# Performance work log

Measured on AMD Instinct MI355X. Metric: run time of the kernel, lower is better.

The kernel has to match this reference:

```python
import jax, jax.numpy as jnp
import numpy as np

B, T, I, H = 64, 512, 512, 512


def setup_inputs() -> dict:
    key = jax.random.key(0)
    ks = jax.random.split(key, 7)
    scale_i = 1.0 / np.sqrt(I)
    scale_h = 1.0 / np.sqrt(H)
    x = jax.random.normal(ks[0], (B, T, I), dtype=jnp.float32)
    h0 = jax.random.normal(ks[1], (B, H), dtype=jnp.float32)
    W_ih = jax.random.normal(ks[2], (3 * H, I), dtype=jnp.float32) * scale_i
    W_hh = jax.random.normal(ks[3], (3 * H, H), dtype=jnp.float32) * scale_h
    b_ih = jax.random.normal(ks[4], (3 * H,), dtype=jnp.float32) * scale_h
    b_hh = jax.random.normal(ks[5], (3 * H,), dtype=jnp.float32) * scale_h
    # ragged lengths, sorted descending (module's slicing logic assumes this)
    lengths = jnp.sort(jax.random.randint(ks[6], (B,), 1, T + 1))[::-1].astype(jnp.int64)
    return {"x": x, "h0": h0, "W_ih": W_ih, "W_hh": W_hh,
            "b_ih": b_ih, "b_hh": b_hh, "lengths": lengths}


def _gru_scan(x, h0, W_ih, W_hh, b_ih, b_hh, lengths):
    # Precompute input projections for all timesteps: [B, T, 3H]
    gi = jnp.einsum('bti,gi->btg', x, W_ih) + b_ih
    lengths = lengths.astype(jnp.int32)

    def step(h, inp):
        gi_t, t = inp  # gi_t: [B, 3H]
        gh = h @ W_hh.T + b_hh  # [B, 3H]
        i_r, i_z, i_n = jnp.split(gi_t, 3, axis=-1)
        h_r, h_z, h_n = jnp.split(gh, 3, axis=-1)
        r = jax.nn.sigmoid(i_r + h_r)
        z = jax.nn.sigmoid(i_z + h_z)
        n = jnp.tanh(i_n + r * h_n)
        h_new = (1.0 - z) * n + z * h
        m = (t < lengths)[:, None]  # ragged mask: valid rows this step
        h_keep = jnp.where(m, h_new, h)        # past-length rows keep last state
        y = jnp.where(m, h_new, 0.0)           # output stays zero past length
        return h_keep, y

    ts = jnp.arange(x.shape[1], dtype=jnp.int32)
    h_final, ys = jax.lax.scan(step, h0, (gi.transpose(1, 0, 2), ts))
    output = ys.transpose(1, 0, 2)  # [B, T, H]
    return output, h_final


def reference(x, h0, W_ih, W_hh, b_ih, b_hh, lengths):
    output, h_final = _gru_scan(x, h0, W_ih, W_hh, b_ih, b_hh, lengths)
    final_state = (h_final[None],)  # (1, B, H), matching unsqueeze(0)
    return output, final_state
```

## Files before the change

kernel.cpp:

```cpp
#include <hip/hip_runtime.h>
#include <stdint.h>

#define Bsz 64
#define Tsz 512
#define HD  512
#define GROUPS 4
#define MEMBERS 16
#define BROWS 16
#define JCH 32
#define NWG (GROUPS*MEMBERS)
#define NTHR 512
#define LROW 520
#define LROWD 260
#define HSLOT (Bsz*HD/2)

typedef __attribute__((ext_vector_type(8))) short bf16x8;
typedef __attribute__((ext_vector_type(4))) float f32x4;
typedef __attribute__((ext_vector_type(4))) uint32_t u32x4;
typedef __attribute__((ext_vector_type(2))) uint32_t u32x2;

#define BAR() asm volatile("s_waitcnt lgkmcnt(0)\n\ts_barrier" ::: "memory")

__device__ __forceinline__ uint32_t f2bf(float f) {
  uint32_t u = __builtin_bit_cast(uint32_t, f);
  return (u + 0x7FFFu + ((u >> 16) & 1u)) >> 16;
}

__device__ __forceinline__ bf16x8 ldwf(const float* __restrict__ W, int row, int k0) {
  const f32x4 a = *reinterpret_cast<const f32x4*>(W + (size_t)row * HD + k0);
  const f32x4 b = *reinterpret_cast<const f32x4*>(W + (size_t)row * HD + k0 + 4);
  bf16x8 r;
  r[0] = (short)f2bf(a.x); r[1] = (short)f2bf(a.y);
  r[2] = (short)f2bf(a.z); r[3] = (short)f2bf(a.w);
  r[4] = (short)f2bf(b.x); r[5] = (short)f2bf(b.y);
  r[6] = (short)f2bf(b.z); r[7] = (short)f2bf(b.w);
  return r;
}

__device__ __forceinline__ void stage_x0(const float* __restrict__ x, int b0,
                                         uint32_t* xl, int tid) {
#pragma unroll
  for (int i = 0; i < 4; ++i) {
    const int fl = tid + i * 512;
    const int row = fl >> 7;
    const int c4 = fl & 127;
    const f32x4 v = *reinterpret_cast<const f32x4*>(
        x + (size_t)(b0 + row) * Tsz * HD + c4 * 4);
    u32x2 w;
    w.x = f2bf(v.x) | (f2bf(v.y) << 16);
    w.y = f2bf(v.z) | (f2bf(v.w) << 16);
    *reinterpret_cast<u32x2*>(xl + row * LROWD + c4 * 2) = w;
  }
}

__global__ void gru_init(const float* __restrict__ h0, uint32_t* __restrict__ flg,
                         uint64_t* __restrict__ hbx) {
  const int i = blockIdx.x * 256 + threadIdx.x;
  if (i < 2 * GROUPS * 16) flg[i] = (i < GROUPS * 16) ? 0xFFFFFFFFu : 0u;
  if (i < HSLOT) {
    const float a = h0[2 * i], b = h0[2 * i + 1];
    hbx[HSLOT + i] = (uint64_t)(f2bf(a) | (f2bf(b) << 16));
    hbx[i] = 0xFFFFFFFF00000000ull;
  }
}

__global__ void __launch_bounds__(NTHR) gru_persist(
    const float* __restrict__ x, const float* __restrict__ h0,
    const float* __restrict__ Wih, const float* __restrict__ Whh,
    const float* __restrict__ bih, const float* __restrict__ bhh,
    const int* __restrict__ lens,
    float* __restrict__ out, float* __restrict__ outh,
    uint32_t* __restrict__ flg, uint64_t* __restrict__ hbx) {
  __shared__ alignas(16) unsigned short x_lds[2][BROWS * LROW];
  __shared__ alignas(16) unsigned short h_lds[BROWS * LROW];
  __shared__ alignas(16) float s_lds[BROWS][4][JCH];

  const int tid = threadIdx.x;
  const int lane = tid & 63;
  const int wv = tid >> 6;
  const int gid = blockIdx.x & 3;
  const int mem = blockIdx.x >> 2;
  const int b0 = gid * BROWS;
  const int j0 = mem * JCH;

  const int grow = tid >> 5;
  const int gj = tid & 31;
  const float br = bih[j0 + gj] + bhh[j0 + gj];
  const float bz = bih[512 + j0 + gj] + bhh[512 + j0 + gj];
  const float bi_n = bih[1024 + j0 + gj];
  const float bh_n = bhh[1024 + j0 + gj];
  float hprev = h0[(size_t)(b0 + grow) * HD + j0 + gj];
  const int lenr = lens[b0 + grow];
  float* const outp = out + (size_t)(b0 + grow) * Tsz * HD + j0 + gj;

  const int q = tid & 127;
  const int r0 = tid >> 7;

  const int xc4 = tid & 127;
  const int xr0 = tid >> 7;
  const float* xbp[4];
#pragma unroll
  for (int i = 0; i < 4; ++i)
    xbp[i] = x + (size_t)(b0 + xr0 + 4 * i) * Tsz * HD + xc4 * 4;

  const int c = lane & 15;
  const int kg = lane >> 4;
  bf16x8 wfa[16], wfb[16];
  if (wv < 4) {
    const int wrow = (wv >> 1) * 512 + j0 + (wv & 1) * 16 + c;
#pragma unroll
    for (int ks = 0; ks < 16; ++ks) {
      const int k0 = ks * 32 + kg * 8;
      wfa[ks] = ldwf(Wih, wrow, k0);
      wfb[ks] = ldwf(Whh, wrow, k0);
    }
  } else if (wv < 6) {
    const int wrow = 1024 + j0 + (wv - 4) * 16 + c;
#pragma unroll
    for (int ks = 0; ks < 16; ++ks) wfa[ks] = ldwf(Wih, wrow, ks * 32 + kg * 8);
  } else {
    const int wrow = 1024 + j0 + (wv - 6) * 16 + c;
#pragma unroll
    for (int ks = 0; ks < 16; ++ks) wfb[ks] = ldwf(Whh, wrow, ks * 32 + kg * 8);
  }

  stage_x0(x, b0, (uint32_t*)&x_lds[0][0], tid);

  f32x4 xr[4];
#pragma unroll
  for (int i = 0; i < 4; ++i)
    xr[i] = *reinterpret_cast<const f32x4*>(xbp[i] + (size_t)1 * HD);

  float o_pend = 0.f;

  __syncthreads();

  for (int t = 0; t < Tsz; ++t) {
    const uint32_t want = (uint32_t)t;
    const uint64_t* bp = hbx + (size_t)((t + 1) & 1) * HSLOT;
    const uint64_t* a0 = bp + (size_t)(b0 + r0) * 256 + q * 2;
    const uint64_t* a1 = a0 + 4 * 256;
    const uint64_t* a2 = a0 + 8 * 256;
    const uint64_t* a3 = a0 + 12 * 256;
    u32x4 d0, d1, d2, d3;

    asm volatile(
        "global_load_dwordx4 %0, %4, off sc0 sc1\n\t"
        "global_load_dwordx4 %1, %5, off sc0 sc1\n\t"
        "global_load_dwordx4 %2, %6, off sc0 sc1\n\t"
        "global_load_dwordx4 %3, %7, off sc0 sc1"
        : "=&v"(d0), "=&v"(d1), "=&v"(d2), "=&v"(d3)
        : "v"(a0), "v"(a1), "v"(a2), "v"(a3)
        : "memory");

    f32x4 acc0 = {0.f, 0.f, 0.f, 0.f}, acc1 = {0.f, 0.f, 0.f, 0.f};
    {
      const unsigned short* xl = &x_lds[t & 1][0];
      if (wv < 6) {
#pragma unroll
        for (int ks = 0; ks < 16; ks += 2) {
          bf16x8 a0f = *reinterpret_cast<const bf16x8*>(xl + c * LROW + ks * 32 + kg * 8);
          bf16x8 a1f = *reinterpret_cast<const bf16x8*>(xl + c * LROW + (ks + 1) * 32 + kg * 8);
          acc0 = __builtin_amdgcn_mfma_f32_16x16x32_bf16(a0f, wfa[ks], acc0, 0, 0, 0);
          acc1 = __builtin_amdgcn_mfma_f32_16x16x32_bf16(a1f, wfa[ks + 1], acc1, 0, 0, 0);
        }
      }
    }

    if (t + 1 < Tsz) {
      uint32_t* xl = (uint32_t*)&x_lds[(t + 1) & 1][0];
#pragma unroll
      for (int i = 0; i < 4; ++i) {
        u32x2 w;
        w.x = f2bf(xr[i].x) | (f2bf(xr[i].y) << 16);
        w.y = f2bf(xr[i].z) | (f2bf(xr[i].w) << 16);
        *reinterpret_cast<u32x2*>(xl + (xr0 + 4 * i) * LROWD + xc4 * 2) = w;
      }
    }

    asm volatile("s_waitcnt vmcnt(0)" ::: "memory");
    __builtin_amdgcn_sched_barrier(0);
    {
      bool ok = (d0[1] == want) & (d0[3] == want) & (d1[1] == want) &
                (d1[3] == want) & (d2[1] == want) & (d2[3] == want) &
                (d3[1] == want) & (d3[3] == want);
      if (!ok) {
        const uint32_t* fl = flg + ((((t + 1) & 1) * GROUPS + gid) << 4);
        for (;;) {
          u32x4 f0, f1, f2, f3;
          asm volatile(
              "global_load_dwordx4 %0, %4, off sc0 sc1\n\t"
              "global_load_dwordx4 %1, %4, off offset:16 sc0 sc1\n\t"
              "global_load_dwordx4 %2, %4, off offset:32 sc0 sc1\n\t"
              "global_load_dwordx4 %3, %4, off offset:48 sc0 sc1\n\t"
              "s_waitcnt vmcnt(0)"
              : "=&v"(f0), "=&v"(f1), "=&v"(f2), "=&v"(f3)
              : "v"(fl)
              : "memory");
          bool fok = true;
#pragma unroll
          for (int i = 0; i < 4; ++i)
            fok &= (f0[i] == want) & (f1[i] == want) & (f2[i] == want) & (f3[i] == want);
          if (fok) break;
        }
        for (;;) {
          asm volatile(
              "global_load_dwordx4 %0, %4, off sc0 sc1\n\t"
              "global_load_dwordx4 %1, %5, off sc0 sc1\n\t"
              "global_load_dwordx4 %2, %6, off sc0 sc1\n\t"
              "global_load_dwordx4 %3, %7, off sc0 sc1\n\t"
              "s_waitcnt vmcnt(0)"
              : "=&v"(d0), "=&v"(d1), "=&v"(d2), "=&v"(d3)
              : "v"(a0), "v"(a1), "v"(a2), "v"(a3)
              : "memory");
          __builtin_amdgcn_sched_barrier(0);
          const bool rok = (d0[1] == want) & (d0[3] == want) & (d1[1] == want) &
                           (d1[3] == want) & (d2[1] == want) & (d2[3] == want) &
                           (d3[1] == want) & (d3[3] == want);
          if (rok) break;
        }
      }
    }
    {
      uint32_t* hd = (uint32_t*)&h_lds[0] + q * 2;
      u32x2 w;
      w.x = d0[0]; w.y = d0[2];
      *reinterpret_cast<u32x2*>(hd + (r0) * LROWD) = w;
      w.x = d1[0]; w.y = d1[2];
      *reinterpret_cast<u32x2*>(hd + (r0 + 4) * LROWD) = w;
      w.x = d2[0]; w.y = d2[2];
      *reinterpret_cast<u32x2*>(hd + (r0 + 8) * LROWD) = w;
      w.x = d3[0]; w.y = d3[2];
      *reinterpret_cast<u32x2*>(hd + (r0 + 12) * LROWD) = w;
    }

    if (t > 0) outp[(size_t)(t - 1) * HD] = o_pend;

    BAR();

    if (t + 2 < Tsz) {
#pragma unroll
      for (int i = 0; i < 4; ++i)
        xr[i] = *reinterpret_cast<const f32x4*>(xbp[i] + (size_t)(t + 2) * HD);
    }

    {
      const unsigned short* hl = &h_lds[0];
      if (wv < 4 || wv >= 6) {
#pragma unroll
        for (int ks = 0; ks < 16; ks += 2) {
          bf16x8 a0f = *reinterpret_cast<const bf16x8*>(hl + c * LROW + ks * 32 + kg * 8);
          bf16x8 a1f = *reinterpret_cast<const bf16x8*>(hl + c * LROW + (ks + 1) * 32 + kg * 8);
          acc0 = __builtin_amdgcn_mfma_f32_16x16x32_bf16(a0f, wfb[ks], acc0, 0, 0, 0);
          acc1 = __builtin_amdgcn_mfma_f32_16x16x32_bf16(a1f, wfb[ks + 1], acc1, 0, 0, 0);
        }
      }
      const f32x4 acc = acc0 + acc1;
      const int slot = (wv < 4) ? (wv >> 1) : ((wv < 6) ? 2 : 3);
      const int col = (wv & 1) * 16 + c;
#pragma unroll
      for (int qq = 0; qq < 4; ++qq) s_lds[kg * 4 + qq][slot][col] = acc[qq];
    }
    BAR();

    {
      const float sr = s_lds[grow][0][gj] + br;
      const float sz = s_lds[grow][1][gj] + bz;
      const float si = s_lds[grow][2][gj] + bi_n;
      const float sh = s_lds[grow][3][gj] + bh_n;
      const float r = 1.f / (1.f + __expf(-sr));
      const float z = 1.f / (1.f + __expf(-sz));
      const float n = tanhf(si + r * sh);
      const float hnew = (1.f - z) * n + z * hprev;
      const bool m = (t < lenr);
      const float hk = m ? hnew : hprev;
      const uint32_t ub = f2bf(hk);
      const uint32_t ot = __shfl_xor(ub, 1);
      if ((t + 1 < Tsz) && ((lane & 1) == 0)) {
        const uint32_t word = ub | (ot << 16);
        const uint64_t pkt = ((uint64_t)(uint32_t)(t + 1) << 32) | (uint64_t)word;
        __hip_atomic_store(hbx + (size_t)(t & 1) * HSLOT + (size_t)(b0 + grow) * 256 +
                               ((j0 + gj) >> 1),
                           pkt, __ATOMIC_RELAXED, __HIP_MEMORY_SCOPE_AGENT);
      }
      if ((t + 1 < Tsz) && (tid == 0)) {
        __hip_atomic_store(flg + (((t & 1) * GROUPS + gid) << 4) + mem,
                           (uint32_t)(t + 1), __ATOMIC_RELAXED,
                           __HIP_MEMORY_SCOPE_AGENT);
      }
      o_pend = m ? hnew : 0.f;
      hprev = hk;
    }
  }

  outp[(size_t)(Tsz - 1) * HD] = o_pend;
  outh[(size_t)(b0 + grow) * HD + j0 + gj] = hprev;
}

extern "C" void kernel_launch(void* const* d_in, const int* in_sizes, int n_in,
                              void* d_out, int out_size, void* d_ws, size_t ws_size,
                              hipStream_t stream) {
  const float* x = (const float*)d_in[0];
  const float* h0 = (const float*)d_in[1];
  const float* Wih = (const float*)d_in[2];
  const float* Whh = (const float*)d_in[3];
  const float* bih = (const float*)d_in[4];
  const float* bhh = (const float*)d_in[5];
  const int* lens = (const int*)d_in[6];
  float* out = (float*)d_out;
  float* outh = out + (size_t)Bsz * Tsz * HD;

  uint32_t* flg = (uint32_t*)d_ws;
  uint64_t* hbx = (uint64_t*)((char*)d_ws + 512);

  gru_init<<<64, 256, 0, stream>>>(h0, flg, hbx);
  gru_persist<<<NWG, NTHR, 0, stream>>>(x, h0, Wih, Whh, bih, bhh, lens,
                                        out, outh, flg, hbx);
}
```

Before: 1.606 ms.

## Prefetch group flags across steps and load hidden state after flag check

The per-step handshake changes. The group flag words are prefetched at the end of the previous step, and the flag check now runs before the packed hidden-state loads are issued. The data loads overlap with the x-tile bf16 conversion and the next x prefetch, which moves ahead of the barrier, and a partial vmcnt wait releases them early. The output is written directly each step instead of being deferred. The goal is to hide global-memory latency in the recurrent sync. The risk is that a stale flag prefetch forces an extra poll followed by a serialized data-load round trip.

Result: faster. 1.472 ms (-8.3%).

```diff
diff --git a/kernel.cpp b/kernel.cpp
--- a/kernel.cpp
+++ b/kernel.cpp
@@ -131,27 +131,23 @@
   for (int i = 0; i < 4; ++i)
     xr[i] = *reinterpret_cast<const f32x4*>(xbp[i] + (size_t)1 * HD);
 
-  float o_pend = 0.f;
+  u32x4 pf0, pf1, pf2, pf3;
+  {
+    const uint32_t* fl = flg + ((1 * GROUPS + gid) << 4);
+    asm volatile(
+        "global_load_dwordx4 %0, %4, off sc0 sc1\n\t"
+        "global_load_dwordx4 %1, %4, off offset:16 sc0 sc1\n\t"
+        "global_load_dwordx4 %2, %4, off offset:32 sc0 sc1\n\t"
+        "global_load_dwordx4 %3, %4, off offset:48 sc0 sc1"
+        : "=&v"(pf0), "=&v"(pf1), "=&v"(pf2), "=&v"(pf3)
+        : "v"(fl)
+        : "memory");
+  }
 
   __syncthreads();
 
   for (int t = 0; t < Tsz; ++t) {
     const uint32_t want = (uint32_t)t;
-    const uint64_t* bp = hbx + (size_t)((t + 1) & 1) * HSLOT;
-    const uint64_t* a0 = bp + (size_t)(b0 + r0) * 256 + q * 2;
-    const uint64_t* a1 = a0 + 4 * 256;
-    const uint64_t* a2 = a0 + 8 * 256;
-    const uint64_t* a3 = a0 + 12 * 256;
-    u32x4 d0, d1, d2, d3;
-
-    asm volatile(
-        "global_load_dwordx4 %0, %4, off sc0 sc1\n\t"
-        "global_load_dwordx4 %1, %5, off sc0 sc1\n\t"
-        "global_load_dwordx4 %2, %6, off sc0 sc1\n\t"
-        "global_load_dwordx4 %3, %7, off sc0 sc1"
-        : "=&v"(d0), "=&v"(d1), "=&v"(d2), "=&v"(d3)
-        : "v"(a0), "v"(a1), "v"(a2), "v"(a3)
-        : "memory");
 
     f32x4 acc0 = {0.f, 0.f, 0.f, 0.f}, acc1 = {0.f, 0.f, 0.f, 0.f};
     {
@@ -167,23 +163,13 @@
       }
     }
 
-    if (t + 1 < Tsz) {
-      uint32_t* xl = (uint32_t*)&x_lds[(t + 1) & 1][0];
-#pragma unroll
-      for (int i = 0; i < 4; ++i) {
-        u32x2 w;
-        w.x = f2bf(xr[i].x) | (f2bf(xr[i].y) << 16);
-        w.y = f2bf(xr[i].z) | (f2bf(xr[i].w) << 16);
-        *reinterpret_cast<u32x2*>(xl + (xr0 + 4 * i) * LROWD + xc4 * 2) = w;
-      }
-    }
-
     asm volatile("s_waitcnt vmcnt(0)" ::: "memory");
     __builtin_amdgcn_sched_barrier(0);
     {
-      bool ok = (d0[1] == want) & (d0[3] == want) & (d1[1] == want) &
-                (d1[3] == want) & (d2[1] == want) & (d2[3] == want) &
-                (d3[1] == want) & (d3[3] == want);
+      bool ok = true;
+#pragma unroll
+      for (int i = 0; i < 4; ++i)
+        ok &= (pf0[i] == want) & (pf1[i] == want) & (pf2[i] == want) & (pf3[i] == want);
       if (!ok) {
         const uint32_t* fl = flg + ((((t + 1) & 1) * GROUPS + gid) << 4);
         for (;;) {
@@ -197,29 +183,69 @@
               : "=&v"(f0), "=&v"(f1), "=&v"(f2), "=&v"(f3)
               : "v"(fl)
               : "memory");
+          __builtin_amdgcn_sched_barrier(0);
           bool fok = true;
 #pragma unroll
           for (int i = 0; i < 4; ++i)
             fok &= (f0[i] == want) & (f1[i] == want) & (f2[i] == want) & (f3[i] == want);
           if (fok) break;
         }
-        for (;;) {
-          asm volatile(
-              "global_load_dwordx4 %0, %4, off sc0 sc1\n\t"
-              "global_load_dwordx4 %1, %5, off sc0 sc1\n\t"
-              "global_load_dwordx4 %2, %6, off sc0 sc1\n\t"
-              "global_load_dwordx4 %3, %7, off sc0 sc1\n\t"
-              "s_waitcnt vmcnt(0)"
-              : "=&v"(d0), "=&v"(d1), "=&v"(d2), "=&v"(d3)
-              : "v"(a0), "v"(a1), "v"(a2), "v"(a3)
-              : "memory");
-          __builtin_amdgcn_sched_barrier(0);
-          const bool rok = (d0[1] == want) & (d0[3] == want) & (d1[1] == want) &
-                           (d1[3] == want) & (d2[1] == want) & (d2[3] == want) &
-                           (d3[1] == want) & (d3[3] == want);
-          if (rok) break;
-        }
-      }
+      }
+    }
+
+    const uint64_t* bp = hbx + (size_t)((t + 1) & 1) * HSLOT;
+    const uint64_t* a0 = bp + (size_t)(b0 + r0) * 256 + q * 2;
+    const uint64_t* a1 = a0 + 4 * 256;
+    const uint64_t* a2 = a0 + 8 * 256;
+    const uint64_t* a3 = a0 + 12 * 256;
+    u32x4 d0, d1, d2, d3;
+    asm volatile(
+        "global_load_dwordx4 %0, %4, off sc0 sc1\n\t"
+        "global_load_dwordx4 %1, %5, off sc0 sc1\n\t"
+        "global_load_dwordx4 %2, %6, off sc0 sc1\n\t"
+        "global_load_dwordx4 %3, %7, off sc0 sc1"
+        : "=&v"(d0), "=&v"(d1), "=&v"(d2), "=&v"(d3)
+        : "v"(a0), "v"(a1), "v"(a2), "v"(a3)
+        : "memory");
+
+    if (t + 1 < Tsz) {
+      uint32_t* xl = (uint32_t*)&x_lds[(t + 1) & 1][0];
+#pragma unroll
+      for (int i = 0; i < 4; ++i) {
+        u32x2 w;
+        w.x = f2bf(xr[i].x) | (f2bf(xr[i].y) << 16);
+        w.y = f2bf(xr[i].z) | (f2bf(xr[i].w) << 16);
+        *reinterpret_cast<u32x2*>(xl + (xr0 + 4 * i) * LROWD + xc4 * 2) = w;
+      }
+    }
+
+    if (t + 2 < Tsz) {
+#pragma unroll
+      for (int i = 0; i < 4; ++i)
+        xr[i] = *reinterpret_cast<const f32x4*>(xbp[i] + (size_t)(t + 2) * HD);
+    }
+
+    if (t + 2 < Tsz) {
+      asm volatile("s_waitcnt vmcnt(4)" ::: "memory");
+    } else {
+      asm volatile("s_waitcnt vmcnt(0)" ::: "memory");
+    }
+    __builtin_amdgcn_sched_barrier(0);
+    for (;;) {
+      const bool rok = (d0[1] == want) & (d0[3] == want) & (d1[1] == want) &
+                       (d1[3] == want) & (d2[1] == want) & (d2[3] == want) &
+                       (d3[1] == want) & (d3[3] == want);
+      if (rok) break;
+      asm volatile(
+          "global_load_dwordx4 %0, %4, off sc0 sc1\n\t"
+          "global_load_dwordx4 %1, %5, off sc0 sc1\n\t"
+          "global_load_dwordx4 %2, %6, off sc0 sc1\n\t"
+          "global_load_dwordx4 %3, %7, off sc0 sc1\n\t"
+          "s_waitcnt vmcnt(0)"
+          : "=&v"(d0), "=&v"(d1), "=&v"(d2), "=&v"(d3)
+          : "v"(a0), "v"(a1), "v"(a2), "v"(a3)
+          : "memory");
+      __builtin_amdgcn_sched_barrier(0);
     }
     {
       uint32_t* hd = (uint32_t*)&h_lds[0] + q * 2;
@@ -234,15 +260,7 @@
       *reinterpret_cast<u32x2*>(hd + (r0 + 12) * LROWD) = w;
     }
 
-    if (t > 0) outp[(size_t)(t - 1) * HD] = o_pend;
-
     BAR();
-
-    if (t + 2 < Tsz) {
-#pragma unroll
-      for (int i = 0; i < 4; ++i)
-        xr[i] = *reinterpret_cast<const f32x4*>(xbp[i] + (size_t)(t + 2) * HD);
-    }
 
     {
       const unsigned short* hl = &h_lds[0];
@@ -288,12 +306,22 @@
                            (uint32_t)(t + 1), __ATOMIC_RELAXED,
                            __HIP_MEMORY_SCOPE_AGENT);
       }
-      o_pend = m ? hnew : 0.f;
+      outp[(size_t)t * HD] = m ? hnew : 0.f;
       hprev = hk;
-    }
-  }
-
-  outp[(size_t)(Tsz - 1) * HD] = o_pend;
+      if (t + 1 < Tsz) {
+        const uint32_t* fl = flg + (((t & 1) * GROUPS + gid) << 4);
+        asm volatile(
+            "global_load_dwordx4 %0, %4, off sc0 sc1\n\t"
+            "global_load_dwordx4 %1, %4, off offset:16 sc0 sc1\n\t"
+            "global_load_dwordx4 %2, %4, off offset:32 sc0 sc1\n\t"
+            "global_load_dwordx4 %3, %4, off offset:48 sc0 sc1"
+            : "=&v"(pf0), "=&v"(pf1), "=&v"(pf2), "=&v"(pf3)
+            : "v"(fl)
+            : "memory");
+      }
+    }
+  }
+
   outh[(size_t)(b0 + grow) * HD + j0 + gj] = hprev;
 }
 
```

## Halve workgroups per batch group and double hidden-column chunk per workgroup

Applied to the files above, without the earlier changes.

Each batch group is now covered by 8 workgroups of 1024 threads, each owning 64 hidden columns, instead of 16 workgroups of 512 threads with 32 columns each. The per-step synchronisation is also restructured: a flag poll over the 8 member flags runs first, then the h-state reload, replacing the speculative load with a fallback path. Fewer participants in the cross-workgroup barrier should cut synchronisation latency per timestep. The costs are more MFMA work per workgroup and a doubled block size, plus an always-taken flag wait before the data load. The remaining code that writes flags and h must also match the new member count.

Result: slower. 3.684 ms (+129.4%).

```diff
diff --git a/kernel.cpp b/kernel.cpp
--- a/kernel.cpp
+++ b/kernel.cpp
@@ -5,11 +5,11 @@
 #define Tsz 512
 #define HD  512
 #define GROUPS 4
-#define MEMBERS 16
+#define MEMBERS 8
 #define BROWS 16
-#define JCH 32
+#define JCH 64
 #define NWG (GROUPS*MEMBERS)
-#define NTHR 512
+#define NTHR 1024
 #define LROW 520
 #define LROWD 260
 #define HSLOT (Bsz*HD/2)
@@ -40,8 +40,8 @@
 __device__ __forceinline__ void stage_x0(const float* __restrict__ x, int b0,
                                          uint32_t* xl, int tid) {
 #pragma unroll
-  for (int i = 0; i < 4; ++i) {
-    const int fl = tid + i * 512;
+  for (int i = 0; i < 2; ++i) {
+    const int fl = tid + i * 1024;
     const int row = fl >> 7;
     const int c4 = fl & 127;
     const f32x4 v = *reinterpret_cast<const f32x4*>(
@@ -83,8 +83,8 @@
   const int b0 = gid * BROWS;
   const int j0 = mem * JCH;
 
-  const int grow = tid >> 5;
-  const int gj = tid & 31;
+  const int grow = tid >> 6;
+  const int gj = tid & 63;
   const float br = bih[j0 + gj] + bhh[j0 + gj];
   const float bz = bih[512 + j0 + gj] + bhh[512 + j0 + gj];
   const float bi_n = bih[1024 + j0 + gj];
@@ -98,37 +98,37 @@
 
   const int xc4 = tid & 127;
   const int xr0 = tid >> 7;
-  const float* xbp[4];
-#pragma unroll
-  for (int i = 0; i < 4; ++i)
-    xbp[i] = x + (size_t)(b0 + xr0 + 4 * i) * Tsz * HD + xc4 * 4;
+  const float* xbp[2];
+#pragma unroll
+  for (int i = 0; i < 2; ++i)
+    xbp[i] = x + (size_t)(b0 + xr0 + 8 * i) * Tsz * HD + xc4 * 4;
 
   const int c = lane & 15;
   const int kg = lane >> 4;
   bf16x8 wfa[16], wfb[16];
-  if (wv < 4) {
-    const int wrow = (wv >> 1) * 512 + j0 + (wv & 1) * 16 + c;
+  if (wv < 8) {
+    const int wrow = (wv >> 2) * 512 + j0 + (wv & 3) * 16 + c;
 #pragma unroll
     for (int ks = 0; ks < 16; ++ks) {
       const int k0 = ks * 32 + kg * 8;
       wfa[ks] = ldwf(Wih, wrow, k0);
       wfb[ks] = ldwf(Whh, wrow, k0);
     }
-  } else if (wv < 6) {
-    const int wrow = 1024 + j0 + (wv - 4) * 16 + c;
+  } else if (wv < 12) {
+    const int wrow = 1024 + j0 + (wv - 8) * 16 + c;
 #pragma unroll
     for (int ks = 0; ks < 16; ++ks) wfa[ks] = ldwf(Wih, wrow, ks * 32 + kg * 8);
   } else {
-    const int wrow = 1024 + j0 + (wv - 6) * 16 + c;
+    const int wrow = 1024 + j0 + (wv - 12) * 16 + c;
 #pragma unroll
     for (int ks = 0; ks < 16; ++ks) wfb[ks] = ldwf(Whh, wrow, ks * 32 + kg * 8);
   }
 
   stage_x0(x, b0, (uint32_t*)&x_lds[0][0], tid);
 
-  f32x4 xr[4];
-#pragma unroll
-  for (int i = 0; i < 4; ++i)
+  f32x4 xr[2];
+#pragma unroll
+  for (int i = 0; i < 2; ++i)
     xr[i] = *reinterpret_cast<const f32x4*>(xbp[i] + (size_t)1 * HD);
 
   float o_pend = 0.f;
@@ -137,26 +137,11 @@
 
   for (int t = 0; t < Tsz; ++t) {
     const uint32_t want = (uint32_t)t;
-    const uint64_t* bp = hbx + (size_t)((t + 1) & 1) * HSLOT;
-    const uint64_t* a0 = bp + (size_t)(b0 + r0) * 256 + q * 2;
-    const uint64_t* a1 = a0 + 4 * 256;
-    const uint64_t* a2 = a0 + 8 * 256;
-    const uint64_t* a3 = a0 + 12 * 256;
-    u32x4 d0, d1, d2, d3;
-
-    asm volatile(
-        "global_load_dwordx4 %0, %4, off sc0 sc1\n\t"
-        "global_load_dwordx4 %1, %5, off sc0 sc1\n\t"
-        "global_load_dwordx4 %2, %6, off sc0 sc1\n\t"
-        "global_load_dwordx4 %3, %7, off sc0 sc1"
-        : "=&v"(d0), "=&v"(d1), "=&v"(d2), "=&v"(d3)
-        : "v"(a0), "v"(a1), "v"(a2), "v"(a3)
-        : "memory");
 
     f32x4 acc0 = {0.f, 0.f, 0.f, 0.f}, acc1 = {0.f, 0.f, 0.f, 0.f};
     {
       const unsigned short* xl = &x_lds[t & 1][0];
-      if (wv < 6) {
+      if (wv < 12) {
 #pragma unroll
         for (int ks = 0; ks < 16; ks += 2) {
           bf16x8 a0f = *reinterpret_cast<const bf16x8*>(xl + c * LROW + ks * 32 + kg * 8);
@@ -170,68 +155,57 @@
     if (t + 1 < Tsz) {
       uint32_t* xl = (uint32_t*)&x_lds[(t + 1) & 1][0];
 #pragma unroll
-      for (int i = 0; i < 4; ++i) {
+      for (int i = 0; i < 2; ++i) {
         u32x2 w;
         w.x = f2bf(xr[i].x) | (f2bf(xr[i].y) << 16);
         w.y = f2bf(xr[i].z) | (f2bf(xr[i].w) << 16);
-        *reinterpret_cast<u32x2*>(xl + (xr0 + 4 * i) * LROWD + xc4 * 2) = w;
-      }
-    }
-
-    asm volatile("s_waitcnt vmcnt(0)" ::: "memory");
-    __builtin_amdgcn_sched_barrier(0);
-    {
-      bool ok = (d0[1] == want) & (d0[3] == want) & (d1[1] == want) &
-                (d1[3] == want) & (d2[1] == want) & (d2[3] == want) &
-                (d3[1] == want) & (d3[3] == want);
-      if (!ok) {
-        const uint32_t* fl = flg + ((((t + 1) & 1) * GROUPS + gid) << 4);
-        for (;;) {
-          u32x4 f0, f1, f2, f3;
-          asm volatile(
-              "global_load_dwordx4 %0, %4, off sc0 sc1\n\t"
-              "global_load_dwordx4 %1, %4, off offset:16 sc0 sc1\n\t"
-              "global_load_dwordx4 %2, %4, off offset:32 sc0 sc1\n\t"
-              "global_load_dwordx4 %3, %4, off offset:48 sc0 sc1\n\t"
-              "s_waitcnt vmcnt(0)"
-              : "=&v"(f0), "=&v"(f1), "=&v"(f2), "=&v"(f3)
-              : "v"(fl)
-              : "memory");
-          bool fok = true;
-#pragma unroll
-          for (int i = 0; i < 4; ++i)
-            fok &= (f0[i] == want) & (f1[i] == want) & (f2[i] == want) & (f3[i] == want);
-          if (fok) break;
-        }
-        for (;;) {
-          asm volatile(
-              "global_load_dwordx4 %0, %4, off sc0 sc1\n\t"
-              "global_load_dwordx4 %1, %5, off sc0 sc1\n\t"
-              "global_load_dwordx4 %2, %6, off sc0 sc1\n\t"
-              "global_load_dwordx4 %3, %7, off sc0 sc1\n\t"
-              "s_waitcnt vmcnt(0)"
-              : "=&v"(d0), "=&v"(d1), "=&v"(d2), "=&v"(d3)
-              : "v"(a0), "v"(a1), "v"(a2), "v"(a3)
-              : "memory");
-          __builtin_amdgcn_sched_barrier(0);
-          const bool rok = (d0[1] == want) & (d0[3] == want) & (d1[1] == want) &
-                           (d1[3] == want) & (d2[1] == want) & (d2[3] == want) &
-                           (d3[1] == want) & (d3[3] == want);
-          if (rok) break;
-        }
-      }
-    }
-    {
+        *reinterpret_cast<u32x2*>(xl + (xr0 + 8 * i) * LROWD + xc4 * 2) = w;
+      }
+    }
+
+    {
+      const uint32_t* fl = flg + ((((t + 1) & 1) * GROUPS + gid) << 4);
+      for (;;) {
+        u32x4 f0, f1;
+        asm volatile(
+            "global_load_dwordx4 %0, %2, off sc0 sc1\n\t"
+            "global_load_dwordx4 %1, %2, off offset:16 sc0 sc1\n\t"
+            "s_waitcnt vmcnt(0)"
+            : "=&v"(f0), "=&v"(f1)
+            : "v"(fl)
+            : "memory");
+        __builtin_amdgcn_sched_barrier(0);
+        bool fok = true;
+#pragma unroll
+        for (int i = 0; i < 4; ++i) fok &= (f0[i] == want) & (f1[i] == want);
+        if (fok) break;
+      }
+    }
+
+    {
+      const uint64_t* bp = hbx + (size_t)((t + 1) & 1) * HSLOT;
+      const uint64_t* a0 = bp + (size_t)(b0 + r0) * 256 + q * 2;
+      const uint64_t* a1 = a0 + 8 * 256;
+      u32x4 d0, d1;
+      for (;;) {
+        asm volatile(
+            "global_load_dwordx4 %0, %2, off sc0 sc1\n\t"
+            "global_load_dwordx4 %1, %3, off sc0 sc1\n\t"
+            "s_waitcnt vmcnt(0)"
+            : "=&v"(d0), "=&v"(d1)
+            : "v"(a0), "v"(a1)
+            : "memory");
+        __builtin_amdgcn_sched_barrier(0);
+        const bool rok = (d0[1] == want) & (d0[3] == want) &
+                         (d1[1] == want) & (d1[3] == want);
+        if (rok) break;
+      }
       uint32_t* hd = (uint32_t*)&h_lds[0] + q * 2;
       u32x2 w;
       w.x = d0[0]; w.y = d0[2];
       *reinterpret_cast<u32x2*>(hd + (r0) * LROWD) = w;
       w.x = d1[0]; w.y = d1[2];
-      *reinterpret_cast<u32x2*>(hd + (r0 + 4) * LROWD) = w;
-      w.x = d2[0]; w.y = d2[2];
       *reinterpret_cast<u32x2*>(hd + (r0 + 8) * LROWD) = w;
-      w.x = d3[0]; w.y = d3[2];
-      *reinterpret_cast<u32x2*>(hd + (r0 + 12) * LROWD) = w;
     }
 
     if (t > 0) outp[(size_t)(t - 1) * HD] = o_pend;
@@ -240,13 +214,13 @@
 
     if (t + 2 < Tsz) {
 #pragma unroll
-      for (int i = 0; i < 4; ++i)
+      for (int i = 0; i < 2; ++i)
         xr[i] = *reinterpret_cast<const f32x4*>(xbp[i] + (size_t)(t + 2) * HD);
     }
 
     {
       const unsigned short* hl = &h_lds[0];
-      if (wv < 4 || wv >= 6) {
+      if (wv < 8 || wv >= 12) {
 #pragma unroll
         for (int ks = 0; ks < 16; ks += 2) {
           bf16x8 a0f = *reinterpret_cast<const bf16x8*>(hl + c * LROW + ks * 32 + kg * 8);
@@ -256,8 +230,8 @@
         }
       }
       const f32x4 acc = acc0 + acc1;
-      const int slot = (wv < 4) ? (wv >> 1) : ((wv < 6) ? 2 : 3);
-      const int col = (wv & 1) * 16 + c;
+      const int slot = wv >> 2;
+      const int col = (wv & 3) * 16 + c;
 #pragma unroll
       for (int qq = 0; qq < 4; ++qq) s_lds[kg * 4 + qq][slot][col] = acc[qq];
     }
```
